# Performance work log

Measured on AMD Instinct MI355X. Metric: run time of the kernel, lower is better.

## Reference

```python
import jax, jax.numpy as jnp
import numpy as np

NUM_EDGES = 131072  # number of hyperedges (segments)


def setup_inputs() -> dict:
    key = jax.random.key(0)
    k_x, k_idx, k_w1, k_w2 = jax.random.split(key, 4)
    NNZ, D_IN, D_HID, D_OUT = 2097152, 128, 512, 128
    x = jax.random.normal(k_x, (NNZ, D_IN), dtype=jnp.float32)
    hyperedge_index = jax.random.randint(k_idx, (2, NNZ), 0, NUM_EDGES).astype(jnp.int64)
    # MLP params (num_layers=2: Linear(d_in,hid) -> ReLU -> Linear(hid,d_out))
    W1 = jax.random.normal(k_w1, (D_IN, D_HID), dtype=jnp.float32) / np.sqrt(D_IN)
    b1 = jnp.zeros((D_HID,), dtype=jnp.float32)
    W2 = jax.random.normal(k_w2, (D_HID, D_OUT), dtype=jnp.float32) / np.sqrt(D_HID)
    b2 = jnp.zeros((D_OUT,), dtype=jnp.float32)
    return {"x": x, "hyperedge_index": hyperedge_index, "W1": W1, "b1": b1, "W2": W2, "b2": b2}


def reference(x, hyperedge_index, W1, b1, W2, b2):
    seg = hyperedge_index[1]  # hyperedge id per incidence entry
    # scatter_mean over dim 0: segmented sum / count (empty segments -> 0)
    sums = jax.ops.segment_sum(x, seg, num_segments=NUM_EDGES)          # [E, d_in]
    cnt = jax.ops.segment_sum(jnp.ones((x.shape[0],), x.dtype), seg, num_segments=NUM_EDGES)
    mean = sums / jnp.maximum(cnt, 1.0)[:, None]                        # [E, d_in]
    # MLP: Linear -> ReLU -> Linear (norm_type='None', dropout inactive)
    h = jax.nn.relu(mean @ W1 + b1)
    return h @ W2 + b2
```

## Files before the change

### kernel.cpp

```cpp
#include <hip/hip_runtime.h>

#define E_EDGES 131072
#define D_IN 128
#define D_HID 512
#define D_OUT 128

typedef __bf16 bf16x8 __attribute__((ext_vector_type(8)));
typedef float f32x4 __attribute__((ext_vector_type(4)));

__device__ __forceinline__ unsigned short f2bf(float f) {
    unsigned int u = __float_as_uint(f);
    unsigned int r = (u + 0x7FFFu + ((u >> 16) & 1u)) >> 16;
    return (unsigned short)r;
}

__global__ void zero_kernel(int* __restrict__ cnt) {
    int i = blockIdx.x * blockDim.x + threadIdx.x;
    ((int4*)cnt)[i] = make_int4(0, 0, 0, 0);
}

__global__ void hist_kernel(const int* __restrict__ seg, int* __restrict__ cnt, int nnz) {
    int i = blockIdx.x * blockDim.x + threadIdx.x;
    if (i * 4 < nnz) {
        int4 s = ((const int4*)seg)[i];
        atomicAdd(&cnt[s.x], 1);
        atomicAdd(&cnt[s.y], 1);
        atomicAdd(&cnt[s.z], 1);
        atomicAdd(&cnt[s.w], 1);
    }
}

__global__ void blocksum_kernel(const int* __restrict__ cnt, int* __restrict__ bsum) {
    __shared__ int wsum[4];
    const int b = blockIdx.x, t = threadIdx.x;
    int4 c = ((const int4*)cnt)[b * 256 + t];
    int s = c.x + c.y + c.z + c.w;
    for (int d = 32; d; d >>= 1) s += __shfl_down(s, d);
    if ((t & 63) == 0) wsum[t >> 6] = s;
    __syncthreads();
    if (t == 0) bsum[b] = wsum[0] + wsum[1] + wsum[2] + wsum[3];
}

__global__ void bscan_kernel(const int* __restrict__ bsum, int* __restrict__ bpre,
                             int* __restrict__ off_last) {
    const int l = threadIdx.x;
    int a = bsum[2 * l], b = bsum[2 * l + 1];
    int s = a + b;
    for (int d = 1; d < 64; d <<= 1) {
        int u = __shfl_up(s, d);
        if (l >= d) s += u;
    }
    int excl = s - (a + b);
    bpre[2 * l] = excl;
    bpre[2 * l + 1] = excl + a;
    if (l == 63) off_last[0] = s;
}

__global__ void scan2_kernel(const int* __restrict__ cnt, const int* __restrict__ bpre,
                             int* __restrict__ off, int* __restrict__ cur) {
    __shared__ int wsum[4];
    const int b = blockIdx.x, t = threadIdx.x;
    const int gid = b * 256 + t;
    int4 c = ((const int4*)cnt)[gid];
    const int s = c.x + c.y + c.z + c.w;
    const int lane = t & 63, w = t >> 6;
    int incl = s;
    for (int d = 1; d < 64; d <<= 1) {
        int u = __shfl_up(incl, d);
        if (lane >= d) incl += u;
    }
    if (lane == 63) wsum[w] = incl;
    __syncthreads();
    int woff = 0;
    for (int i = 0; i < w; ++i) woff += wsum[i];
    const int base = bpre[b] + woff + (incl - s);
    int4 o;
    o.x = base;
    o.y = base + c.x;
    o.z = base + c.x + c.y;
    o.w = base + c.x + c.y + c.z;
    ((int4*)off)[gid] = o;
    ((int4*)cur)[gid] = o;
}

__global__ void fill_kernel(const int* __restrict__ seg, int* __restrict__ cur,
                            int* __restrict__ csr, int nnz) {
    int i = blockIdx.x * blockDim.x + threadIdx.x;
    if (i * 4 < nnz) {
        int4 s = ((const int4*)seg)[i];
        int p0 = atomicAdd(&cur[s.x], 1);
        int p1 = atomicAdd(&cur[s.y], 1);
        int p2 = atomicAdd(&cur[s.z], 1);
        int p3 = atomicAdd(&cur[s.w], 1);
        csr[p0] = i * 4;
        csr[p1] = i * 4 + 1;
        csr[p2] = i * 4 + 2;
        csr[p3] = i * 4 + 3;
    }
}

__global__ void convw_kernel(const float* __restrict__ W1, const float* __restrict__ W2,
                             unsigned short* __restrict__ w1b, unsigned short* __restrict__ w2b) {
    int i = blockIdx.x * blockDim.x + threadIdx.x;
    if (i < D_IN * D_HID) {
        int n = i >> 7, k = i & 127;
        w1b[i] = f2bf(W1[(size_t)k * D_HID + n]);
    } else {
        int i2 = i - D_IN * D_HID;
        int n = i2 >> 9, k = i2 & 511;
        w2b[i2] = f2bf(W2[(size_t)k * D_OUT + n]);
    }
}

__global__ __launch_bounds__(256) void fused_kernel(
    const float* __restrict__ x, const int* __restrict__ csr,
    const int* __restrict__ off, const unsigned short* __restrict__ w1b,
    const unsigned short* __restrict__ w2b, const float* __restrict__ b1,
    const float* __restrict__ b2, float* __restrict__ out)
{
    __shared__ unsigned short mean_lds[64 * 128];
    __shared__ unsigned short hslice[4][16 * 32];

    const int tid  = threadIdx.x;
    const int lane = tid & 63;
    const int w    = tid >> 6;
    const int tile = blockIdx.x;
    const int row0 = w * 16;

    const int c  = lane & 31;
    const int rr = lane >> 5;
    const char* xb = (const char*)x + c * 16;

    int oreg = off[tile * 64 + row0 + (lane < 17 ? lane : 16)];

    for (int el = 0; el < 16; ++el) {
        const int row = row0 + el;
        const int beg = __shfl(oreg, el);
        const int end = __shfl(oreg, el + 1);
        const int n = end - beg;
        const int* ce = csr + beg;
        f32x4 a0 = {0.f, 0.f, 0.f, 0.f}, a1 = a0, a2 = a0, a3 = a0;
        int j = 0;
        for (; j + 8 <= n; j += 8) {
            int i0 = ce[j + 0 + rr];
            int i1 = ce[j + 2 + rr];
            int i2 = ce[j + 4 + rr];
            int i3 = ce[j + 6 + rr];
            f32x4 v0 = *(const f32x4*)(xb + (size_t)i0 * 512);
            f32x4 v1 = *(const f32x4*)(xb + (size_t)i1 * 512);
            f32x4 v2 = *(const f32x4*)(xb + (size_t)i2 * 512);
            f32x4 v3 = *(const f32x4*)(xb + (size_t)i3 * 512);
            a0 += v0; a1 += v1; a2 += v2; a3 += v3;
        }
        for (; j < n; j += 2) {
            const int jr = j + rr;
            const bool valid = jr < n;
            int idx = ce[valid ? jr : n - 1];
            f32x4 v = *(const f32x4*)(xb + (size_t)idx * 512);
            if (valid) a0 += v;
        }
        f32x4 tot = (a0 + a1) + (a2 + a3);
        tot[0] += __shfl_xor(tot[0], 32);
        tot[1] += __shfl_xor(tot[1], 32);
        tot[2] += __shfl_xor(tot[2], 32);
        tot[3] += __shfl_xor(tot[3], 32);
        const float scale = 1.0f / (float)(n > 0 ? n : 1);
        if (lane < 32) {
            unsigned int d0 = (unsigned)f2bf(tot[0] * scale) | ((unsigned)f2bf(tot[1] * scale) << 16);
            unsigned int d1 = (unsigned)f2bf(tot[2] * scale) | ((unsigned)f2bf(tot[3] * scale) << 16);
            unsigned int byte = ((unsigned)(row * 256 + c * 8)) ^ ((unsigned)(row & 7) << 4);
            uint2* p = (uint2*)((char*)mean_lds + byte);
            *p = make_uint2(d0, d1);
        }
    }

    const int lrow = lane & 15;
    const int lgrp = lane >> 4;

    bf16x8 afrag[4];
#pragma unroll
    for (int kk = 0; kk < 4; ++kk) {
        int row = row0 + lrow;
        unsigned int byte = ((unsigned)(row * 256 + kk * 64 + lgrp * 16)) ^ ((unsigned)(row & 7) << 4);
        afrag[kk] = *(const bf16x8*)((const char*)mean_lds + byte);
    }

    const f32x4 fzero = {0.f, 0.f, 0.f, 0.f};
    f32x4 acc2[8];
#pragma unroll
    for (int t = 0; t < 8; ++t) acc2[t] = fzero;

    unsigned short* hs = &hslice[w][0];

    for (int ntp = 0; ntp < 16; ++ntp) {
#pragma unroll
        for (int half = 0; half < 2; ++half) {
            const int nt = ntp * 2 + half;
            f32x4 acc = fzero;
#pragma unroll
            for (int kk = 0; kk < 4; ++kk) {
                const bf16x8 b = *(const bf16x8*)(w1b + (size_t)(nt * 16 + lrow) * 128 + kk * 32 + lgrp * 8);
                acc = __builtin_amdgcn_mfma_f32_16x16x32_bf16(afrag[kk], b, acc, 0, 0, 0);
            }
            const int hcol = nt * 16 + lrow;
            const float bias = b1[hcol];
#pragma unroll
            for (int r = 0; r < 4; ++r) {
                float v = acc[r] + bias;
                v = fmaxf(v, 0.f);
                const int rowD = lgrp * 4 + r;
                const int klocal = half * 16 + lrow;
                unsigned int byte = ((unsigned)(rowD * 64 + klocal * 2)) ^ ((unsigned)(rowD & 3) << 4);
                *(unsigned short*)((char*)hs + byte) = f2bf(v);
            }
        }
        {
            unsigned int byte = ((unsigned)(lrow * 64 + lgrp * 16)) ^ ((unsigned)(lrow & 3) << 4);
            const bf16x8 a2 = *(const bf16x8*)((const char*)hs + byte);
#pragma unroll
            for (int nt2 = 0; nt2 < 8; ++nt2) {
                const bf16x8 b = *(const bf16x8*)(w2b + (size_t)(nt2 * 16 + lrow) * 512 + ntp * 32 + lgrp * 8);
                acc2[nt2] = __builtin_amdgcn_mfma_f32_16x16x32_bf16(a2, b, acc2[nt2], 0, 0, 0);
            }
        }
    }

#pragma unroll
    for (int nt2 = 0; nt2 < 8; ++nt2) {
        const int col = nt2 * 16 + lrow;
        const float bias = b2[col];
#pragma unroll
        for (int r = 0; r < 4; ++r) {
            const int row = tile * 64 + row0 + lgrp * 4 + r;
            out[(size_t)row * 128 + col] = acc2[nt2][r] + bias;
        }
    }
}

extern "C" void kernel_launch(void* const* d_in, const int* in_sizes, int n_in,
                              void* d_out, int out_size, void* d_ws, size_t ws_size,
                              hipStream_t stream)
{
    const float* x  = (const float*)d_in[0];
    const int* hyper = (const int*)d_in[1];
    const float* W1 = (const float*)d_in[2];
    const float* b1 = (const float*)d_in[3];
    const float* W2 = (const float*)d_in[4];
    const float* b2 = (const float*)d_in[5];
    const int nnz = in_sizes[0] / D_IN;
    const int* seg = hyper + nnz;

    char* ws = (char*)d_ws;
    int* cnt  = (int*)(ws + 0x000000);
    int* off  = (int*)(ws + 0x080000);
    int* cur  = (int*)(ws + 0x100100);
    int* csr  = (int*)(ws + 0x180100);
    unsigned short* w1b = (unsigned short*)(ws + 0x980100);
    unsigned short* w2b = (unsigned short*)(ws + 0x9A0100);
    int* bsum = (int*)(ws + 0x9C0100);
    int* bpre = (int*)(ws + 0x9C0300);
    float* out = (float*)d_out;

    hipLaunchKernelGGL(zero_kernel, dim3(128), dim3(256), 0, stream, cnt);
    hipLaunchKernelGGL(hist_kernel, dim3(nnz / 1024), dim3(256), 0, stream, seg, cnt, nnz);
    hipLaunchKernelGGL(blocksum_kernel, dim3(128), dim3(256), 0, stream, cnt, bsum);
    hipLaunchKernelGGL(bscan_kernel, dim3(1), dim3(64), 0, stream, bsum, bpre, off + E_EDGES);
    hipLaunchKernelGGL(scan2_kernel, dim3(128), dim3(256), 0, stream, cnt, bpre, off, cur);
    hipLaunchKernelGGL(fill_kernel, dim3(nnz / 1024), dim3(256), 0, stream, seg, cur, csr, nnz);
    hipLaunchKernelGGL(convw_kernel, dim3((D_IN * D_HID + D_HID * D_OUT) / 256), dim3(256), 0,
                       stream, W1, W2, w1b, w2b);
    hipLaunchKernelGGL(fused_kernel, dim3(E_EDGES / 64), dim3(256), 0, stream,
                       x, csr, off, w1b, w2b, b1, b2, out);
}
```

Before: 775.1 us.

## Split fused gather+MLP kernel into separate gather and GEMM kernels

Unfuses the segment-mean gather from the MLP GEMM. The gather kernel now writes bf16 means to a global workspace buffer, and a separate GEMM kernel reads them back. The gather loop uses 8 independent accumulators with per-slot bounds checks and nontemporal loads, which puts more loads in flight and avoids polluting the cache with x. This frees the memory-bound gather from the GEMM's register and LDS footprint, which should raise occupancy. The cost is a 32MB round-trip through global memory plus an extra kernel launch.

```diff
diff --git a/kernel.cpp b/kernel.cpp
--- a/kernel.cpp
+++ b/kernel.cpp
@@ -112,15 +112,10 @@
     }
 }
 
-__global__ __launch_bounds__(256) void fused_kernel(
+__global__ __launch_bounds__(256) void gather_kernel(
     const float* __restrict__ x, const int* __restrict__ csr,
-    const int* __restrict__ off, const unsigned short* __restrict__ w1b,
-    const unsigned short* __restrict__ w2b, const float* __restrict__ b1,
-    const float* __restrict__ b2, float* __restrict__ out)
+    const int* __restrict__ off, unsigned short* __restrict__ meanb)
 {
-    __shared__ unsigned short mean_lds[64 * 128];
-    __shared__ unsigned short hslice[4][16 * 32];
-
     const int tid  = threadIdx.x;
     const int lane = tid & 63;
     const int w    = tid >> 6;
@@ -139,27 +134,24 @@
         const int end = __shfl(oreg, el + 1);
         const int n = end - beg;
         const int* ce = csr + beg;
-        f32x4 a0 = {0.f, 0.f, 0.f, 0.f}, a1 = a0, a2 = a0, a3 = a0;
-        int j = 0;
-        for (; j + 8 <= n; j += 8) {
-            int i0 = ce[j + 0 + rr];
-            int i1 = ce[j + 2 + rr];
-            int i2 = ce[j + 4 + rr];
-            int i3 = ce[j + 6 + rr];
-            f32x4 v0 = *(const f32x4*)(xb + (size_t)i0 * 512);
-            f32x4 v1 = *(const f32x4*)(xb + (size_t)i1 * 512);
-            f32x4 v2 = *(const f32x4*)(xb + (size_t)i2 * 512);
-            f32x4 v3 = *(const f32x4*)(xb + (size_t)i3 * 512);
-            a0 += v0; a1 += v1; a2 += v2; a3 += v3;
-        }
-        for (; j < n; j += 2) {
-            const int jr = j + rr;
-            const bool valid = jr < n;
-            int idx = ce[valid ? jr : n - 1];
-            f32x4 v = *(const f32x4*)(xb + (size_t)idx * 512);
-            if (valid) a0 += v;
-        }
-        f32x4 tot = (a0 + a1) + (a2 + a3);
+        f32x4 a0 = {0.f, 0.f, 0.f, 0.f};
+        f32x4 a1 = a0, a2 = a0, a3 = a0, a4 = a0, a5 = a0, a6 = a0, a7 = a0;
+        for (int j = 0; j < n; j += 16) {
+#define GSLOT(k, acc)                                                        \
+            {                                                                \
+                const int jj = j + 2 * (k) + rr;                             \
+                if (jj < n) {                                                \
+                    const int idx = ce[jj];                                  \
+                    f32x4 v = __builtin_nontemporal_load(                    \
+                        (const f32x4*)(xb + (size_t)idx * 512));             \
+                    acc += v;                                                \
+                }                                                            \
+            }
+            GSLOT(0, a0) GSLOT(1, a1) GSLOT(2, a2) GSLOT(3, a3)
+            GSLOT(4, a4) GSLOT(5, a5) GSLOT(6, a6) GSLOT(7, a7)
+#undef GSLOT
+        }
+        f32x4 tot = ((a0 + a1) + (a2 + a3)) + ((a4 + a5) + (a6 + a7));
         tot[0] += __shfl_xor(tot[0], 32);
         tot[1] += __shfl_xor(tot[1], 32);
         tot[2] += __shfl_xor(tot[2], 32);
@@ -168,11 +160,24 @@
         if (lane < 32) {
             unsigned int d0 = (unsigned)f2bf(tot[0] * scale) | ((unsigned)f2bf(tot[1] * scale) << 16);
             unsigned int d1 = (unsigned)f2bf(tot[2] * scale) | ((unsigned)f2bf(tot[3] * scale) << 16);
-            unsigned int byte = ((unsigned)(row * 256 + c * 8)) ^ ((unsigned)(row & 7) << 4);
-            uint2* p = (uint2*)((char*)mean_lds + byte);
-            *p = make_uint2(d0, d1);
-        }
-    }
+            *(uint2*)((char*)meanb + (size_t)row * 256 + (size_t)tile * 16384 + c * 8) =
+                make_uint2(d0, d1);
+        }
+    }
+}
+
+__global__ __launch_bounds__(256) void gemm_kernel(
+    const unsigned short* __restrict__ meanb, const unsigned short* __restrict__ w1b,
+    const unsigned short* __restrict__ w2b, const float* __restrict__ b1,
+    const float* __restrict__ b2, float* __restrict__ out)
+{
+    __shared__ unsigned short hslice[4][16 * 32];
+
+    const int tid  = threadIdx.x;
+    const int lane = tid & 63;
+    const int w    = tid >> 6;
+    const int tile = blockIdx.x;
+    const int row0 = w * 16;
 
     const int lrow = lane & 15;
     const int lgrp = lane >> 4;
@@ -180,9 +185,8 @@
     bf16x8 afrag[4];
 #pragma unroll
     for (int kk = 0; kk < 4; ++kk) {
-        int row = row0 + lrow;
-        unsigned int byte = ((unsigned)(row * 256 + kk * 64 + lgrp * 16)) ^ ((unsigned)(row & 7) << 4);
-        afrag[kk] = *(const bf16x8*)((const char*)mean_lds + byte);
+        const int row = tile * 64 + row0 + lrow;
+        afrag[kk] = *(const bf16x8*)(meanb + (size_t)row * 128 + kk * 32 + lgrp * 8);
     }
 
     const f32x4 fzero = {0.f, 0.f, 0.f, 0.f};
@@ -259,6 +263,7 @@
     unsigned short* w2b = (unsigned short*)(ws + 0x9A0100);
     int* bsum = (int*)(ws + 0x9C0100);
     int* bpre = (int*)(ws + 0x9C0300);
+    unsigned short* meanb = (unsigned short*)(ws + 0xA00000);
     float* out = (float*)d_out;
 
     hipLaunchKernelGGL(zero_kernel, dim3(128), dim3(256), 0, stream, cnt);
@@ -269,6 +274,8 @@
     hipLaunchKernelGGL(fill_kernel, dim3(nnz / 1024), dim3(256), 0, stream, seg, cur, csr, nnz);
     hipLaunchKernelGGL(convw_kernel, dim3((D_IN * D_HID + D_HID * D_OUT) / 256), dim3(256), 0,
                        stream, W1, W2, w1b, w2b);
-    hipLaunchKernelGGL(fused_kernel, dim3(E_EDGES / 64), dim3(256), 0, stream,
-                       x, csr, off, w1b, w2b, b1, b2, out);
-}
+    hipLaunchKernelGGL(gather_kernel, dim3(E_EDGES / 64), dim3(256), 0, stream,
+                       x, csr, off, meanb);
+    hipLaunchKernelGGL(gemm_kernel, dim3(E_EDGES / 64), dim3(256), 0, stream,
+                       meanb, w1b, w2b, b1, b2, out);
+}
```

New measurement: 787.9 us. No clear change (+1.7%).
